# Optimization experiments

Measured on AMD Instinct MI355X. Metric: run time of the kernel, lower is better.

The kernel has to match this reference:

```python
import jax, jax.numpy as jnp
from jax import lax
import numpy as np

B, C, H, W = 64, 1, 256, 256
NUM_BINS = 50
SCALE = 32  # eval-mode scale in the original forward
SENT = H * W  # sentinel label for background


def setup_inputs() -> dict:
    key = jax.random.key(0)
    # Smooth, blob-like attention maps in [0,1] (low-freq random field upsampled),
    # mimicking real attention maps so connected components are compact blobs.
    base = jax.random.uniform(key, (B, C, 16, 16), dtype=jnp.float32)
    att = jax.image.resize(base, (B, C, H, W), method='linear')
    att = jnp.clip(att, 0.0, 0.999)
    return {"att_map": att}


def _histogram_threshold(flat):  # flat: [B, H*W] in [0,1]
    # cv2.calcHist with 50 bins on [0,1]: bin i covers [i/50,(i+1)/50)
    idx = jnp.clip((flat * NUM_BINS).astype(jnp.int32), 0, NUM_BINS - 1)
    counts = jax.vmap(lambda i: jnp.bincount(i, length=NUM_BINS))(idx)  # [B,50]
    ind_max = jnp.argmax(counts, axis=1)  # [B]
    bins = jnp.arange(NUM_BINS)
    # second peak strictly after the global peak (his[ind_max+1:].argmax()+ind_max+1)
    masked = jnp.where(bins[None, :] > ind_max[:, None], counts, -1)
    ind_sec = jnp.argmax(masked, axis=1)  # [B]
    return ind_sec.astype(flat.dtype) / NUM_BINS  # [B]


def _connected_components(fg):  # fg: [H,W] bool -> int32 root labels
    # Min-label propagation over 4-neighborhood until fixpoint
    lab0 = jnp.where(fg, jnp.arange(SENT, dtype=jnp.int32).reshape(H, W),
                     jnp.int32(SENT))

    def nbr_min(l):
        big = jnp.full_like(l, SENT)
        dn = jnp.concatenate([l[1:], big[:1]], axis=0)
        up = jnp.concatenate([big[:1], l[:-1]], axis=0)
        rt = jnp.concatenate([l[:, 1:], big[:, :1]], axis=1)
        lf = jnp.concatenate([big[:, :1], l[:, :-1]], axis=1)
        m = jnp.minimum(jnp.minimum(up, dn), jnp.minimum(lf, rt))
        return jnp.where(fg, jnp.minimum(l, m), jnp.int32(SENT))

    def cond(c):
        return c[1]

    def body(c):
        l = c[0]
        nl = nbr_min(l)
        return (nl, jnp.any(nl != l))

    lab, _ = lax.while_loop(cond, body, (lab0, jnp.array(True)))
    return lab


def _suppression_mask(att_map):
    # Returns (suppress_mask [B,1,H,W] bool, exponent [B,1,H,W] float).
    a = att_map[:, 0]  # [B,H,W]
    thr = _histogram_threshold(a.reshape(B, -1))  # [B]
    fg = a > thr[:, None, None]  # binary map (att > thresold)
    labels = jax.vmap(_connected_components)(fg)  # [B,H,W] int32
    # area of each component (connected-component analogue of contourArea)
    areas = jax.vmap(
        lambda l, f: jax.ops.segment_sum(f.astype(jnp.float32).ravel(),
                                         l.ravel(), num_segments=SENT + 1)
    )(labels, fg)  # [B, H*W+1]
    area_px = jax.vmap(lambda ar, l: ar[l])(areas, labels)  # [B,H,W]
    # eval path: value = get_att_value(area) = area**exp with exp=0.5;
    # suppressed pixels become att ** (1/value)
    expnt = 1.0 / jnp.sqrt(jnp.maximum(area_px, 1.0))
    return fg[:, None], expnt[:, None]


def reference(att_map):
    bin_size = max(H, W) // SCALE
    if bin_size < 5:  # module skips small maps untouched
        return att_map
    suppress, expnt = _suppression_mask(att_map)
    safe = jnp.where(suppress, att_map, 1.0)  # avoid pow at 0 under where
    return jnp.where(suppress, safe ** expnt, att_map)
```

## Files before the change

kernel.cpp:

```cpp
#include <hip/hip_runtime.h>
#include <math.h>

#define BATCH 64
#define HH 256
#define WW 256
#define HW 65536
#define NPIX (BATCH * HW)
#define NBINS 50
#define SENT_P 0x7FFFFFFF

#define TW 64
#define TH 64
#define TN (TW * TH)
#define TILES_X (WW / TW)
#define TILES_PER_IMG 16
#define LIST_STRIDE 32768

__device__ __forceinline__ int aload(const int* p) {
    return __hip_atomic_load(p, __ATOMIC_RELAXED, __HIP_MEMORY_SCOPE_AGENT);
}
__device__ __forceinline__ void astore(int* p, int v) {
    __hip_atomic_store(p, v, __ATOMIC_RELAXED, __HIP_MEMORY_SCOPE_AGENT);
}

__device__ __forceinline__ int runstart64(unsigned long long m, int c) {
    unsigned long long sh = (~m) << (63 - c);
    return sh ? (c - __clzll(sh) + 1) : 0;
}
__device__ __forceinline__ int runlen64(unsigned long long m, int c) {
    unsigned long long sh = ~(m >> c);
    return sh ? (__ffsll(sh) - 1) : 64;
}
__device__ __forceinline__ void wave_argmax(int& bv, int& bi) {
#pragma unroll
    for (int off = 32; off > 0; off >>= 1) {
        int ov = __shfl_xor(bv, off);
        int oi = __shfl_xor(bi, off);
        if (ov > bv || (ov == bv && oi < bi)) { bv = ov; bi = oi; }
    }
}

__global__ void k_hist(const float* __restrict__ att, int* __restrict__ histp,
                       int* __restrict__ rootcnt) {
    __shared__ int h[NBINS];
    const int b = blockIdx.y, c = blockIdx.x, t = threadIdx.x;
    if (c == 0 && t == 0) rootcnt[b] = 0;
    if (t < NBINS) h[t] = 0;
    __syncthreads();
    const float4* src = (const float4*)(att + (size_t)b * HW) + c * 2048;
    for (int i = t; i < 2048; i += 256) {
        float4 v = src[i];
        atomicAdd(&h[min((int)(v.x * 50.0f), 49)], 1);
        atomicAdd(&h[min((int)(v.y * 50.0f), 49)], 1);
        atomicAdd(&h[min((int)(v.z * 50.0f), 49)], 1);
        atomicAdd(&h[min((int)(v.w * 50.0f), 49)], 1);
    }
    __syncthreads();
    if (t < NBINS) histp[(b * 8 + c) * 64 + t] = h[t];
}

__device__ __forceinline__ void lunite(int* lp, int a, int b) {
    int x = a, p = lp[x];
    while (p != x) { int gp = lp[p]; if (gp != p) lp[x] = gp; x = gp; p = lp[x]; }
    int ra = x;
    x = b; p = lp[x];
    while (p != x) { int gp = lp[p]; if (gp != p) lp[x] = gp; x = gp; p = lp[x]; }
    int rb = x;
    while (ra != rb) {
        int lo = min(ra, rb), hi = max(ra, rb);
        int old = atomicMin(&lp[hi], lo);
        if (old == hi) return;
        x = lo; p = lp[x];
        while (p != x) { int gp = lp[p]; if (gp != p) lp[x] = gp; x = gp; p = lp[x]; }
        ra = x;
        x = old; p = lp[x];
        while (p != x) { int gp = lp[p]; if (gp != p) lp[x] = gp; x = gp; p = lp[x]; }
        rb = x;
    }
}
__device__ __forceinline__ int lfindm(int* lp, int x) {
    while (true) {
        int p = lp[x] & 0xFFFF;
        if (p == x) return x;
        int gp = lp[p] & 0xFFFF;
        if (gp != p) lp[x] = gp;
        x = gp;
    }
}

__global__ __launch_bounds__(256)
void k_init_cc(const float* __restrict__ att, const int* __restrict__ histp,
               int* parent, int* __restrict__ cnt, int* __restrict__ list,
               int* __restrict__ rootcnt) {
    __shared__ int lp[TN];
    __shared__ unsigned long long msk[TH];
    const int tile = blockIdx.x;
    const int b = blockIdx.y;
    const int t = threadIdx.x;
    const int wv = t >> 6, ln = t & 63;
    const int tr0 = (tile / TILES_X) * TH;
    const int tc0 = (tile % TILES_X) * TW;
    const float* A = att + (size_t)b * HW;

    int h_ln = 0;
    if (ln < NBINS)
        for (int c = 0; c < 8; ++c) h_ln += histp[(b * 8 + c) * 64 + ln];
    int bv = (ln < NBINS) ? h_ln : -1, bi = ln;
    wave_argmax(bv, bi);
    const int ind_max = bi;
    int bv2 = (ln < NBINS && ln > ind_max) ? h_ln : -1, bi2 = ln;
    wave_argmax(bv2, bi2);
    const double tv = (double)bi2 / 50.0;

    for (int k = 0; k < 16; ++k) {
        int r = wv + 4 * k;
        float x = A[(tr0 + r) * WW + tc0 + ln];
        bool fg = (double)x > tv;
        unsigned long long m = __ballot(fg);
        if (ln == 0) msk[r] = m;
        if (fg && (ln == 0 || !((m >> (ln - 1)) & 1ull)))
            lp[r * TW + ln] = r * TW + ln;
    }
    __syncthreads();

    for (int k = 0; k < 16; ++k) {
        int r = wv + 4 * k;
        if (r >= TH - 1) continue;
        unsigned long long m0 = msk[r], m1 = msk[r + 1];
        unsigned long long ov = m0 & m1;
        if (((ov >> ln) & 1ull) && (ln == 0 || !((ov >> (ln - 1)) & 1ull)))
            lunite(lp, r * TW + runstart64(m0, ln),
                       (r + 1) * TW + runstart64(m1, ln));
    }
    __syncthreads();

    for (int k = 0; k < 16; ++k) {
        int r = wv + 4 * k;
        unsigned long long m = msk[r];
        if (((m >> ln) & 1ull) && (ln == 0 || !((m >> (ln - 1)) & 1ull))) {
            int L = runlen64(m, ln);
            int root = lfindm(lp, r * TW + ln);
            atomicAdd(&lp[root], L << 16);
        }
    }
    __syncthreads();

    int* P = parent + (size_t)b * HW;
    for (int i = t; i < TN / 4; i += 256) {
        int r = i >> 4, c4 = (i & 15) * 4;
        unsigned long long m = msk[r];
        int w[4];
#pragma unroll
        for (int j = 0; j < 4; ++j) {
            int c = c4 + j, l = r * TW + c;
            if (!((m >> c) & 1ull)) { w[j] = SENT_P; continue; }
            int node = r * TW + runstart64(m, c);
            int root = lfindm(lp, node);
            int groot = (tr0 + (root >> 6)) * WW + tc0 + (root & (TW - 1));
            w[j] = groot;
            if (l == root) {
                int size = lp[root] >> 16;
                cnt[(size_t)b * HW + groot] = 0;
                int idx = atomicAdd(&rootcnt[b], 1);
                list[b * LIST_STRIDE + idx] = groot | ((size - 1) << 16);
            }
        }
        *(int4*)(P + (tr0 + r) * WW + tc0 + c4) = make_int4(w[0], w[1], w[2], w[3]);
    }
}

__device__ __forceinline__ int findroot_h(int* P, int x) {
    int p = aload(P + x);
    while (p != x) {
        int gp = aload(P + p);
        astore(P + x, gp);
        x = gp; p = aload(P + x);
    }
    return x;
}
__device__ __forceinline__ void unite(int* P, int a, int b) {
    int ra = findroot_h(P, a);
    int rb = findroot_h(P, b);
    while (ra != rb) {
        int lo = min(ra, rb), hi = max(ra, rb);
        int old = atomicMin(&P[hi], lo);
        if (old == hi) return;
        ra = findroot_h(P, lo);
        rb = findroot_h(P, old);
    }
}
__global__ void k_bmerge(int* parent) {
    int g = blockIdx.x * blockDim.x + threadIdx.x;
    if (g >= BATCH * 1536) return;
    int b = g / 1536, e = g % 1536;
    int* P = parent + (size_t)b * HW;
    int l, m;
    if (e < 768) {
        int k = e / 256, row = e & 255;
        l = row * WW + (TW - 1 + TW * k); m = l + 1;
    } else {
        int e2 = e - 768;
        int k = e2 / 256, col = e2 & 255;
        l = (TH - 1 + TH * k) * WW + col; m = l + WW;
    }
    if (aload(P + l) != SENT_P && aload(P + m) != SENT_P) unite(P, l, m);
}

__global__ void k_acc(const int* __restrict__ parent, int* __restrict__ cnt,
                      const int* __restrict__ list, const int* __restrict__ rootcnt) {
    int g = blockIdx.x * blockDim.x + threadIdx.x;
    int b = g / LIST_STRIDE, i = g - b * LIST_STRIDE;
    if (b >= BATCH || i >= rootcnt[b]) return;
    int e = list[b * LIST_STRIDE + i];
    int x = e & 0xFFFF;
    int size = (e >> 16) + 1;
    const int* P = parent + (size_t)b * HW;
    int p = P[x];
    while (p != x) { x = p; p = P[x]; }
    atomicAdd(&cnt[(size_t)b * HW + x], size);
}

__global__ void k_final(const float* __restrict__ att, const int* __restrict__ parent,
                        const int* __restrict__ cnt, float* __restrict__ out) {
    int g = blockIdx.x * blockDim.x + threadIdx.x;
    int base = g * 4;
    if (base >= NPIX) return;
    const int* P = parent + (base & ~(HW - 1));
    const int* C = cnt + (base & ~(HW - 1));
    float4 v = ((const float4*)att)[g];
    int4 pv = ((const int4*)parent)[g];
    int vv[4] = {pv.x, pv.y, pv.z, pv.w};
    float xs[4] = {v.x, v.y, v.z, v.w};
    float ys[4];
#pragma unroll
    for (int j = 0; j < 4; ++j) {
        float x = xs[j];
        int w = vv[j];
        if (w == SENT_P) { ys[j] = x; continue; }
        int xi = w, p = P[xi];
        while (p != xi) { xi = p; p = P[xi]; }
        float a = (float)C[xi];
        ys[j] = powf(x, 1.0f / sqrtf(a));
    }
    ((float4*)out)[g] = make_float4(ys[0], ys[1], ys[2], ys[3]);
}

__global__ __launch_bounds__(1024)
void k_all(const float* __restrict__ att, float* out) {
    const int b = blockIdx.x;
    const int t = threadIdx.x;
    const float* A = att + (size_t)b * HW;
    int* L = (int*)out + (size_t)b * HW;
    __shared__ int hist[NBINS];
    __shared__ double s_thr;
    __shared__ int s_changed;
    for (int i = t; i < NBINS; i += 1024) hist[i] = 0;
    if (t == 0) s_changed = 0;
    __syncthreads();
    const float4* src4 = (const float4*)A;
    for (int i = t; i < HW / 4; i += 1024) {
        float4 v = src4[i];
        atomicAdd(&hist[min((int)(v.x * 50.0f), 49)], 1);
        atomicAdd(&hist[min((int)(v.y * 50.0f), 49)], 1);
        atomicAdd(&hist[min((int)(v.z * 50.0f), 49)], 1);
        atomicAdd(&hist[min((int)(v.w * 50.0f), 49)], 1);
    }
    __syncthreads();
    if (t == 0) {
        int ind_max = 0, bv = hist[0];
        for (int j = 1; j < NBINS; ++j)
            if (hist[j] > bv) { bv = hist[j]; ind_max = j; }
        int ind_sec = 0, bv2 = -1;
        for (int j = 1; j < NBINS; ++j) {
            int v = (j > ind_max) ? hist[j] : -1;
            if (v > bv2) { bv2 = v; ind_sec = j; }
        }
        s_thr = (double)ind_sec / 50.0;
    }
    __syncthreads();
    const double tv = s_thr;
    for (int i = t; i < HW / 4; i += 1024) {
        float4 v = src4[i];
        int l = i * 4;
        astore(L + l + 0, ((double)v.x > tv) ? (l + 0) : SENT_P);
        astore(L + l + 1, ((double)v.y > tv) ? (l + 1) : SENT_P);
        astore(L + l + 2, ((double)v.z > tv) ? (l + 2) : SENT_P);
        astore(L + l + 3, ((double)v.w > tv) ? (l + 3) : SENT_P);
    }
    __syncthreads();
    for (;;) {
        int changed = 0;
        for (int p = t; p < HW; p += 1024) {
            int v = aload(L + p);
            if (v == SENT_P) continue;
            int m = v;
            int col = p & (WW - 1), row = p >> 8;
            if (col > 0)      m = min(m, aload(L + p - 1));
            if (col < WW - 1) m = min(m, aload(L + p + 1));
            if (row > 0)      m = min(m, aload(L + p - WW));
            if (row < HH - 1) m = min(m, aload(L + p + WW));
            m = min(m, aload(L + m));
            if (m < v) { astore(L + p, m); changed = 1; }
        }
        if (changed) s_changed = 1;
        __syncthreads();
        int ch = s_changed;
        __syncthreads();
        if (!ch) break;
        if (t == 0) s_changed = 0;
        __syncthreads();
    }
    for (int p = t; p < HW; p += 1024) {
        int v = aload(L + p);
        if (v == SENT_P) continue;
        int lo = v & 0xFFFF;
        if (lo != p) atomicAdd((unsigned int*)(L + lo), 0x10000u);
    }
    __syncthreads();
    for (int p = t; p < HW; p += 1024) {
        int v = aload(L + p);
        if (v == SENT_P) continue;
        int lo = v & 0xFFFF;
        if (lo != p) astore(L + p, aload(L + lo));
    }
    __syncthreads();
    for (int p = t; p < HW; p += 1024) {
        float x = A[p];
        unsigned v = (unsigned)aload(L + p);
        float y = x;
        if (v != (unsigned)SENT_P) {
            float a = (float)((v >> 16) + 1u);
            y = powf(x, 1.0f / sqrtf(a));
        }
        out[(size_t)b * HW + p] = y;
    }
}

extern "C" void kernel_launch(void* const* d_in, const int* in_sizes, int n_in,
                              void* d_out, int out_size, void* d_ws, size_t ws_size,
                              hipStream_t stream) {
    const float* att = (const float*)d_in[0];
    float* out = (float*)d_out;
    (void)in_sizes; (void)n_in; (void)out_size;

    const size_t PAR_B  = (size_t)NPIX * 4;
    const size_t CNT_B  = (size_t)NPIX * 4;
    const size_t LIST_B = (size_t)BATCH * LIST_STRIDE * 4;
    const size_t HIST_B = (size_t)BATCH * 8 * 64 * 4;
    if (ws_size < PAR_B + CNT_B + LIST_B + HIST_B + 1024) {
        k_all<<<BATCH, 1024, 0, stream>>>(att, out);
        return;
    }
    int* parent  = (int*)d_ws;
    int* cnt     = (int*)((char*)d_ws + PAR_B);
    int* list    = (int*)((char*)d_ws + PAR_B + CNT_B);
    int* histp   = (int*)((char*)d_ws + PAR_B + CNT_B + LIST_B);
    int* rootcnt = (int*)((char*)d_ws + PAR_B + CNT_B + LIST_B + HIST_B);

    k_hist<<<dim3(8, BATCH), 256, 0, stream>>>(att, histp, rootcnt);
    k_init_cc<<<dim3(TILES_PER_IMG, BATCH), 256, 0, stream>>>(att, histp, parent,
                                                              cnt, list, rootcnt);
    k_bmerge<<<(BATCH * 1536 + 255) / 256, 256, 0, stream>>>(parent);
    k_acc<<<(BATCH * LIST_STRIDE) / 256, 256, 0, stream>>>(parent, cnt, list, rootcnt);
    k_final<<<NPIX / (256 * 4), 256, 0, stream>>>(att, parent, cnt, out);
}
```

Before: 98.31 us.

## Halve CC tile height and build row masks with float4 loads and shared atomicOr

The local connected-component tiles shrink from 64x64 to 64x32. This doubles the number of blocks per image and halves the shared-memory label array, aiming for better occupancy and shorter per-tile union-find work. The foreground bitmask is now built from vectorized float4 loads that OR nibbles into 32-bit shared words, replacing per-row scalar loads with a ballot. In exchange there are more tile boundaries, so the global boundary-merge kernel handles 2560 edges per image instead of 1536, and more roots go through the global union and accumulate passes.

```diff
diff --git a/kernel.cpp b/kernel.cpp
--- a/kernel.cpp
+++ b/kernel.cpp
@@ -10,10 +10,12 @@
 #define SENT_P 0x7FFFFFFF
 
 #define TW 64
-#define TH 64
+#define TH 32
 #define TN (TW * TH)
 #define TILES_X (WW / TW)
-#define TILES_PER_IMG 16
+#define TILES_Y (HH / TH)
+#define TILES_PER_IMG (TILES_X * TILES_Y)
+#define EDGES_PER_IMG 2560
 #define LIST_STRIDE 32768
 
 __device__ __forceinline__ int aload(const int* p) {
@@ -59,23 +61,18 @@
     if (t < NBINS) histp[(b * 8 + c) * 64 + t] = h[t];
 }
 
+__device__ __forceinline__ int lfind(int* lp, int x) {
+    int p = lp[x];
+    while (p != x) { int gp = lp[p]; if (gp != p) lp[x] = gp; x = gp; p = lp[x]; }
+    return x;
+}
 __device__ __forceinline__ void lunite(int* lp, int a, int b) {
-    int x = a, p = lp[x];
-    while (p != x) { int gp = lp[p]; if (gp != p) lp[x] = gp; x = gp; p = lp[x]; }
-    int ra = x;
-    x = b; p = lp[x];
-    while (p != x) { int gp = lp[p]; if (gp != p) lp[x] = gp; x = gp; p = lp[x]; }
-    int rb = x;
+    int ra = lfind(lp, a), rb = lfind(lp, b);
     while (ra != rb) {
         int lo = min(ra, rb), hi = max(ra, rb);
         int old = atomicMin(&lp[hi], lo);
         if (old == hi) return;
-        x = lo; p = lp[x];
-        while (p != x) { int gp = lp[p]; if (gp != p) lp[x] = gp; x = gp; p = lp[x]; }
-        ra = x;
-        x = old; p = lp[x];
-        while (p != x) { int gp = lp[p]; if (gp != p) lp[x] = gp; x = gp; p = lp[x]; }
-        rb = x;
+        ra = lfind(lp, lo); rb = lfind(lp, old);
     }
 }
 __device__ __forceinline__ int lfindm(int* lp, int x) {
@@ -93,7 +90,7 @@
                int* parent, int* __restrict__ cnt, int* __restrict__ list,
                int* __restrict__ rootcnt) {
     __shared__ int lp[TN];
-    __shared__ unsigned long long msk[TH];
+    __shared__ unsigned int msk32[TH * 2];
     const int tile = blockIdx.x;
     const int b = blockIdx.y;
     const int t = threadIdx.x;
@@ -112,21 +109,36 @@
     wave_argmax(bv2, bi2);
     const double tv = (double)bi2 / 50.0;
 
-    for (int k = 0; k < 16; ++k) {
+    if (t < TH * 2) msk32[t] = 0;
+    __syncthreads();
+
+    for (int i = t; i < TN / 4; i += 256) {
+        int r = i >> 4, c4 = (i & 15) * 4;
+        float4 v = *(const float4*)(A + (tr0 + r) * WW + tc0 + c4);
+        unsigned nib = (((double)v.x > tv) ? 1u : 0u)
+                     | (((double)v.y > tv) ? 2u : 0u)
+                     | (((double)v.z > tv) ? 4u : 0u)
+                     | (((double)v.w > tv) ? 8u : 0u);
+        if (nib) atomicOr(&msk32[r * 2 + (c4 >> 5)], nib << (c4 & 31));
+    }
+    __syncthreads();
+
+    for (int k = 0; k < TH / 4; ++k) {
         int r = wv + 4 * k;
-        float x = A[(tr0 + r) * WW + tc0 + ln];
-        bool fg = (double)x > tv;
-        unsigned long long m = __ballot(fg);
-        if (ln == 0) msk[r] = m;
-        if (fg && (ln == 0 || !((m >> (ln - 1)) & 1ull)))
+        unsigned long long m = (unsigned long long)msk32[r * 2]
+                             | ((unsigned long long)msk32[r * 2 + 1] << 32);
+        if (((m >> ln) & 1ull) && (ln == 0 || !((m >> (ln - 1)) & 1ull)))
             lp[r * TW + ln] = r * TW + ln;
     }
     __syncthreads();
 
-    for (int k = 0; k < 16; ++k) {
+    for (int k = 0; k < TH / 4; ++k) {
         int r = wv + 4 * k;
         if (r >= TH - 1) continue;
-        unsigned long long m0 = msk[r], m1 = msk[r + 1];
+        unsigned long long m0 = (unsigned long long)msk32[r * 2]
+                              | ((unsigned long long)msk32[r * 2 + 1] << 32);
+        unsigned long long m1 = (unsigned long long)msk32[(r + 1) * 2]
+                              | ((unsigned long long)msk32[(r + 1) * 2 + 1] << 32);
         unsigned long long ov = m0 & m1;
         if (((ov >> ln) & 1ull) && (ln == 0 || !((ov >> (ln - 1)) & 1ull)))
             lunite(lp, r * TW + runstart64(m0, ln),
@@ -134,9 +146,10 @@
     }
     __syncthreads();
 
-    for (int k = 0; k < 16; ++k) {
+    for (int k = 0; k < TH / 4; ++k) {
         int r = wv + 4 * k;
-        unsigned long long m = msk[r];
+        unsigned long long m = (unsigned long long)msk32[r * 2]
+                             | ((unsigned long long)msk32[r * 2 + 1] << 32);
         if (((m >> ln) & 1ull) && (ln == 0 || !((m >> (ln - 1)) & 1ull))) {
             int L = runlen64(m, ln);
             int root = lfindm(lp, r * TW + ln);
@@ -148,7 +161,8 @@
     int* P = parent + (size_t)b * HW;
     for (int i = t; i < TN / 4; i += 256) {
         int r = i >> 4, c4 = (i & 15) * 4;
-        unsigned long long m = msk[r];
+        unsigned long long m = (unsigned long long)msk32[r * 2]
+                             | ((unsigned long long)msk32[r * 2 + 1] << 32);
         int w[4];
 #pragma unroll
         for (int j = 0; j < 4; ++j) {
@@ -191,8 +205,8 @@
 }
 __global__ void k_bmerge(int* parent) {
     int g = blockIdx.x * blockDim.x + threadIdx.x;
-    if (g >= BATCH * 1536) return;
-    int b = g / 1536, e = g % 1536;
+    if (g >= BATCH * EDGES_PER_IMG) return;
+    int b = g / EDGES_PER_IMG, e = g % EDGES_PER_IMG;
     int* P = parent + (size_t)b * HW;
     int l, m;
     if (e < 768) {
@@ -360,7 +374,7 @@
     k_hist<<<dim3(8, BATCH), 256, 0, stream>>>(att, histp, rootcnt);
     k_init_cc<<<dim3(TILES_PER_IMG, BATCH), 256, 0, stream>>>(att, histp, parent,
                                                               cnt, list, rootcnt);
-    k_bmerge<<<(BATCH * 1536 + 255) / 256, 256, 0, stream>>>(parent);
+    k_bmerge<<<(BATCH * EDGES_PER_IMG + 255) / 256, 256, 0, stream>>>(parent);
     k_acc<<<(BATCH * LIST_STRIDE) / 256, 256, 0, stream>>>(parent, cnt, list, rootcnt);
     k_final<<<NPIX / (256 * 4), 256, 0, stream>>>(att, parent, cnt, out);
 }
```

Result: slower. 102.9 us (+4.7%).
